# Performance work log

Measured on AMD Instinct MI355X. Metric: run time of the kernel, lower is better.

The kernel has to match this reference:

```python
import jax, jax.numpy as jnp
from jax import lax
import numpy as np

B, C, H, W = 8, 192, 56, 56
N = H * W
K_CLUSTERS = 16   # num_centroids
K_NBRS = 9        # kNN neighbors
FACTOR = 2
COUT = C * FACTOR # hidden channels of graph conv
CPE_K = 7         # depthwise CPE kernel (odd)


def setup_inputs() -> dict:
    key = jax.random.key(0)
    ks = jax.random.split(key, 12)
    s = 0.02
    return {
        "x": jax.random.normal(ks[0], (B, C, H, W), jnp.float32),
        "labels": jax.random.randint(ks[1], (B, N), 0, K_CLUSTERS, jnp.int32),
        "cpe_w": jax.random.normal(ks[2], (C, 1, CPE_K, CPE_K), jnp.float32) * s,
        "cpe_b": jnp.zeros((C,), jnp.float32),
        "fc1_w": jax.random.normal(ks[3], (C, C), jnp.float32) * s,
        "fc1_b": jnp.zeros((C,), jnp.float32),
        "nn_v_w": jax.random.normal(ks[4], (2 * C, COUT), jnp.float32) * s,
        "nn_v_b": jnp.zeros((COUT,), jnp.float32),
        "nn_c_w": jax.random.normal(ks[5], (2 * C, COUT), jnp.float32) * s,
        "nn_c_b": jnp.zeros((COUT,), jnp.float32),
        "fc2_w": jax.random.normal(ks[6], (COUT, C), jnp.float32) * s,
        "fc2_b": jnp.zeros((C,), jnp.float32),
    }


def reference(x, labels, cpe_w, cpe_b, fc1_w, fc1_b, nn_v_w, nn_v_b,
              nn_c_w, nn_c_b, fc2_w, fc2_b):
    Bx, Cx, Hx, Wx = x.shape
    n = Hx * Wx
    shortcut = x
    # --- Conditional Position Encoding: depthwise conv + residual ---
    pe = lax.conv_general_dilated(
        x, cpe_w, (1, 1), "SAME", feature_group_count=Cx,
        dimension_numbers=("NCHW", "OIHW", "NCHW"))
    x = pe + cpe_b[None, :, None, None] + x
    # --- fc1: 1x1 conv ---
    xf = jnp.einsum("bchw,cd->bdhw", x, fc1_w) + fc1_b[None, :, None, None]
    xn = xf.reshape(Bx, Cx, n).transpose(0, 2, 1)  # [B,N,C]
    # --- organize_and_map: stable sort nodes by cluster label ---
    order = jnp.argsort(labels, axis=1)            # sorted pos -> orig idx (stable)
    mapping = jnp.argsort(order, axis=1)           # orig idx -> sorted pos
    xs = jnp.take_along_axis(xn, order[:, :, None], axis=1)  # [B,N,C]
    ls = jnp.take_along_axis(labels, order, axis=1)          # [B,N]
    # --- kNN on l2-normalized feats, restricted to same cluster ---
    xe = xs / jnp.maximum(jnp.linalg.norm(xs, axis=-1, keepdims=True), 1e-12)
    sq = jnp.sum(xe * xe, axis=-1)                 # [B,N]
    d2 = sq[:, :, None] + sq[:, None, :] - 2.0 * jnp.einsum("bnc,bmc->bnm", xe, xe)
    same = ls[:, :, None] == ls[:, None, :]        # [B,N,N] cluster mask
    d2 = jnp.where(same, d2, jnp.inf)
    _, nbr = lax.top_k(-d2, K_NBRS)                # [B,N,k] nearest in-cluster
    valid = jnp.take_along_axis(same, nbr, axis=2) # False when cluster < k
    # --- vertex edge conv: max_j MLP([x_i, x_j - x_i]) ---
    xj = jax.vmap(lambda xb, nb: xb[nb])(xs, nbr)  # [B,N,k,C]
    xi = xs[:, :, None, :]
    msg = jnp.concatenate([jnp.broadcast_to(xi, xj.shape), xj - xi], axis=-1)
    h = jax.nn.gelu(msg @ nn_v_w + nn_v_b)         # [B,N,k,COUT]
    h = jnp.where(valid[..., None], h, -jnp.inf)   # self is always valid
    hv = jnp.max(h, axis=2)                        # [B,N,COUT]
    # --- centroid edge conv over cluster centers (fully connected per image) ---
    onehot = (ls[:, :, None] == jnp.arange(K_CLUSTERS)[None, None, :]).astype(xs.dtype)
    cnt = jnp.maximum(onehot.sum(axis=1), 1.0)     # [B,K]
    cen = jnp.einsum("bnk,bnc->bkc", onehot, xs) / cnt[:, :, None]
    ci = cen[:, :, None, :]
    cj = cen[:, None, :, :]
    cmsg = jnp.concatenate(
        [jnp.broadcast_to(ci, (Bx, K_CLUSTERS, K_CLUSTERS, Cx)), cj - ci], axis=-1)
    hc = jnp.max(jax.nn.gelu(cmsg @ nn_c_w + nn_c_b), axis=2)  # [B,K,COUT]
    hcn = jax.vmap(lambda hb, lb: hb[lb])(hc, ls)  # scatter center feat to nodes
    hn = hv + hcn                                  # [B,N,COUT]
    # --- unshuffle back to original raster order ---
    out_nodes = jnp.take_along_axis(hn, mapping[:, :, None], axis=1)
    # --- fc2: 1x1 conv back to C, residual ---
    y = out_nodes @ fc2_w + fc2_b                  # [B,N,C]
    y = y.transpose(0, 2, 1).reshape(Bx, Cx, Hx, Wx)
    return y + shortcut
```

## Files before the change

kernel.cpp:

```cpp
#include <hip/hip_runtime.h>
#include <math.h>

#define NB 8
#define NC 192
#define NH 56
#define NW 56
#define NN 3136
#define NK 16
#define KNB 9
#define NCOUT 384
#define LPMAX 320
#define DSTRIDE 320
#define DSLOT (320 * 320)

#define FLT_INF __builtin_inff()

typedef short s16x8 __attribute__((ext_vector_type(8)));
typedef _Float16 f16x8 __attribute__((ext_vector_type(8)));
typedef float f32x4 __attribute__((ext_vector_type(4)));
typedef unsigned short us8 __attribute__((ext_vector_type(8)));
typedef unsigned short us4 __attribute__((ext_vector_type(4)));

__device__ __forceinline__ float gelu_t(float x) {
    const float k0 = 0.7978845608028654f;
    float u = k0 * (x + 0.044715f * x * x * x);
    float sg = __builtin_amdgcn_rcpf(1.0f + __expf(-2.0f * u));
    return x * sg;
}

__device__ __forceinline__ unsigned short f2bf(float f) {
    unsigned u = __float_as_uint(f);
    u += 0x7fff + ((u >> 16) & 1);
    return (unsigned short)(u >> 16);
}

__device__ __forceinline__ float bf2f(unsigned short h) {
    return __uint_as_float(((unsigned)h) << 16);
}


#define FRONT_CONV_BLOCKS (NB * NC)
#define FRONT_ORDER_BLOCKS (NB * NK)
#define FRONT_WCVT_BLOCKS 288
__global__ __launch_bounds__(256) void front_kernel(
    const float* __restrict__ X, const float* __restrict__ W7, const float* __restrict__ bias,
    unsigned short* __restrict__ xpe,
    const int* __restrict__ labels, int* __restrict__ order, int* __restrict__ mapping,
    int* __restrict__ lsv, int* __restrict__ cntk, int* __restrict__ offk,
    const float* __restrict__ Wf1, const float* __restrict__ Wv, const float* __restrict__ Wf2,
    unsigned short* __restrict__ wf1, unsigned short* __restrict__ wfpmq,
    unsigned short* __restrict__ wfq, unsigned short* __restrict__ wf2) {
    __shared__ float tile[62 * 62];
    __shared__ float wl[49];
    int bid = blockIdx.x;
    int tid = threadIdx.x;
    if (bid < FRONT_CONV_BLOCKS) {
        int bc = (bid & 7) * NC + (bid >> 3);
        int c = bc % NC;
        const float* Xp = X + (size_t)bc * NN;
        if (tid < 49) wl[tid] = W7[(size_t)c * 49 + tid];
        for (int idx = tid; idx < 62 * 62; idx += 256) {
            int ty = idx / 62, tx = idx % 62;
            int gy = ty - 3, gx = tx - 3;
            float v = 0.0f;
            if (gy >= 0 && gy < NH && gx >= 0 && gx < NW) v = Xp[gy * NW + gx];
            tile[idx] = v;
        }
        __syncthreads();
        float cb = bias[c];
        for (int g = tid; g < (NN / 4); g += 256) {
            int y = g / (NW / 4), x0 = (g % (NW / 4)) * 4;
            float a0 = 0.f, a1 = 0.f, a2 = 0.f, a3 = 0.f;
#pragma unroll
            for (int dy = 0; dy < 7; ++dy) {
                const float* tr = &tile[(y + dy) * 62 + x0];
#pragma unroll
                for (int dx = 0; dx < 7; ++dx) {
                    float wv = wl[dy * 7 + dx];
                    a0 += tr[dx] * wv;
                    a1 += tr[dx + 1] * wv;
                    a2 += tr[dx + 2] * wv;
                    a3 += tr[dx + 3] * wv;
                }
            }
            const float* rr = &tile[(y + 3) * 62 + x0 + 3];
            us4 o;
            o[0] = f2bf(a0 + cb + rr[0]);
            o[1] = f2bf(a1 + cb + rr[1]);
            o[2] = f2bf(a2 + cb + rr[2]);
            o[3] = f2bf(a3 + cb + rr[3]);
            *(us4*)(xpe + (size_t)bc * NN + y * NW + x0) = o;
        }
    } else if (bid < FRONT_CONV_BLOCKS + FRONT_ORDER_BLOCKS) {
        if (tid >= 64) return;
        int idx = bid - FRONT_CONV_BLOCKS;
        int b = idx >> 4;
        int k = idx & 15;
        int lane = tid;
        const int* lb = labels + (size_t)b * NN;
        int cntLess = 0, cntEq = 0;
        for (int n0 = 0; n0 < NN; n0 += 64) {
            int lab = lb[n0 + lane] & 15;
            cntLess += __popcll(__ballot(lab < k));
            cntEq += __popcll(__ballot(lab == k));
        }
        int base = cntLess;
        int run = 0;
        for (int n0 = 0; n0 < NN; n0 += 64) {
            int n = n0 + lane;
            int lab = lb[n] & 15;
            bool p = (lab == k);
            unsigned long long mask = __ballot(p);
            int rank = __popcll(mask & ((1ull << lane) - 1ull));
            if (p) {
                int pos = base + run + rank;
                order[b * NN + pos] = n;
                mapping[b * NN + n] = pos;
                lsv[b * NN + pos] = k;
            }
            run += __popcll(mask);
        }
        if (lane == 0) {
            offk[b * NK + k] = base;
            cntk[b * NK + k] = cntEq;
        }
    } else {
        int u = bid - (FRONT_CONV_BLOCKS + FRONT_ORDER_BLOCKS);
        int nt = u % 6, kc = (u / 6) % 12, z = u / 72;
        const float* W;
        unsigned short* Bf;
        int ldw, rowoff, KC, NT;
        bool diff = false;
        if (z == 0) { W = Wf1; Bf = wf1; ldw = NC; rowoff = 0; KC = 6; NT = 3; }
        else if (z == 1) { W = Wv; Bf = wfpmq; ldw = NCOUT; rowoff = 0; KC = 6; NT = 6; diff = true; }
        else if (z == 2) { W = Wv; Bf = wfq; ldw = NCOUT; rowoff = NC; KC = 6; NT = 6; }
        else { W = Wf2; Bf = wf2; ldw = NC; rowoff = 0; KC = 12; NT = 3; }
        if (nt >= NT || kc >= KC) return;
        int c = tid >> 6, l = tid & 63;
        int n = l & 15, q = l >> 4;
        int col = nt * 64 + c * 16 + n;
        int krow = rowoff + kc * 32 + q * 8;
        unsigned short pack[8];
#pragma unroll
        for (int j = 0; j < 8; ++j) {
            float v = W[(size_t)(krow + j) * ldw + col];
            if (diff) v -= W[(size_t)(NC + krow + j) * ldw + col];
            pack[j] = f2bf(v);
        }
        *(us8*)(Bf + ((((size_t)nt * KC + kc) * 4 + c) * 64 + l) * 8) = *(const us8*)pack;
    }
}

__global__ __launch_bounds__(256) void fc1_kernel(const unsigned short* __restrict__ xpe,
                                                  const unsigned short* __restrict__ Bf,
                                                  const float* __restrict__ bias,
                                                  float* __restrict__ xs,
                                                  unsigned short* __restrict__ Cfrag,
                                                  const int* __restrict__ rowmap) {
    int lin = blockIdx.x;
    int b = lin & 7, by = lin >> 3;
    int w = threadIdx.x >> 6, lane = threadIdx.x & 63;
    int sg = by * 4 + w;
    int m = lane & 15, q = lane >> 4;
    int n = by * 64 + w * 16 + m;
    const unsigned short* Xb = xpe + (size_t)b * NC * NN + n;
    f32x4 acc[12] = {};
#pragma unroll
    for (int kc = 0; kc < 6; ++kc) {
        int ch = kc * 32 + q * 8;
        s16x8 a;
#pragma unroll
        for (int j = 0; j < 8; ++j) a[j] = (short)Xb[(size_t)(ch + j) * NN];
#pragma unroll
        for (int ct = 0; ct < 12; ++ct) {
            s16x8 bv = *(const s16x8*)(Bf + ((((size_t)(ct >> 2) * 6 + kc) * 4 + (ct & 3)) * 64 + lane) * 8);
            acc[ct] = __builtin_amdgcn_mfma_f32_16x16x32_bf16(a, bv, acc[ct], 0, 0, 0);
        }
    }
    float* Cb = xs + (size_t)b * NN * NC;
#pragma unroll
    for (int r = 0; r < 4; ++r) {
        int grow = sg * 16 + q * 4 + r;
        int orow = rowmap[(size_t)b * NN + grow];
        int s2 = orow >> 4, m2 = orow & 15;
#pragma unroll
        for (int ct = 0; ct < 12; ++ct) {
            int col = ct * 16 + m;
            float v = acc[ct][r] + bias[col];
            Cb[(size_t)orow * NC + col] = v;
            int kc2 = col >> 5, q2 = (col >> 3) & 3, j2 = col & 7;
            Cfrag[(size_t)b * NN * NC + (((size_t)s2 * 6 + kc2) * 64 + q2 * 16 + m2) * 8 + j2] =
                f2bf(v);
        }
    }
}

template <int KC>
__global__ __launch_bounds__(256) void gemm_mfma_pq(const unsigned short* __restrict__ Af,
                                                    size_t aStride,
                                                    const unsigned short* __restrict__ B1,
                                                    const unsigned short* __restrict__ B2,
                                                    const float* __restrict__ bias,
                                                    unsigned short* __restrict__ PmQ,
                                                    unsigned short* __restrict__ Qh,
                                                    size_t cStride, int ldc) {
    int lin = ((int)blockIdx.z * 49 + blockIdx.y) * 6 + blockIdx.x;
    int b = lin & 7, pos = lin >> 3;
    int bx = pos % 6, by = pos / 6;
    int w = threadIdx.x >> 6, lane = threadIdx.x & 63;
    int sg = by * 4 + w;
    int n0 = bx * 64;
    const unsigned short* Ap = Af + (size_t)b * aStride + ((size_t)sg * KC * 64 + lane) * 8;
    const unsigned short* Bp1 = B1 + ((size_t)bx * KC * 256 + lane) * 8;
    const unsigned short* Bp2 = B2 + ((size_t)bx * KC * 256 + lane) * 8;
    f32x4 acc1[4] = {};
    f32x4 acc2[4] = {};
#pragma unroll
    for (int kc = 0; kc < KC; ++kc) {
        s16x8 a = *(const s16x8*)(Ap + kc * 512);
#pragma unroll
        for (int c = 0; c < 4; ++c) {
            s16x8 b1 = *(const s16x8*)(Bp1 + kc * 2048 + c * 512);
            acc1[c] = __builtin_amdgcn_mfma_f32_16x16x32_bf16(a, b1, acc1[c], 0, 0, 0);
            s16x8 b2 = *(const s16x8*)(Bp2 + kc * 2048 + c * 512);
            acc2[c] = __builtin_amdgcn_mfma_f32_16x16x32_bf16(a, b2, acc2[c], 0, 0, 0);
        }
    }
    int col0 = lane & 15, rq = lane >> 4;
    unsigned short* Pb = PmQ + (size_t)b * cStride;
    unsigned short* Qb = Qh + (size_t)b * cStride;
#pragma unroll
    for (int r = 0; r < 4; ++r) {
        int grow = sg * 16 + rq * 4 + r;
#pragma unroll
        for (int c = 0; c < 4; ++c) {
            int col = n0 + c * 16 + col0;
            Pb[(size_t)grow * ldc + col] = f2bf(acc1[c][r] + bias[col]);
            Qb[(size_t)grow * ldc + col] = f2bf(acc2[c][r]);
        }
    }
}

__global__ __launch_bounds__(384) void xe_cvt_kernel(const float* __restrict__ xs,
                                                     const int* __restrict__ offk,
                                                     const int* __restrict__ cntk,
                                                     _Float16* __restrict__ xef,
                                                     float* __restrict__ sqv) {
    __shared__ float psum[16][25];
    __shared__ float rloc[16];
    int lin = ((int)blockIdx.z * 16 + blockIdx.y) * 20 + blockIdx.x;
    int b = lin & 7, pos = lin >> 3;
    int k = pos / 20, strip = pos % 20;
    int bk = b * NK + k;
    int base = offk[bk], L = cntk[bk];
    if (strip * 16 >= L) return;
    int kc = threadIdx.x >> 6, l = threadIdx.x & 63;
    int m = l & 15, q = l >> 4;
    int rl = strip * 16 + m;
    int row = base + (rl < L ? rl : L - 1);
    const float* src = xs + ((size_t)b * NN + row) * NC + kc * 32 + q * 8;
    float4 v0 = *(const float4*)src;
    float4 v1 = *(const float4*)(src + 4);
    float part = v0.x * v0.x + v0.y * v0.y + v0.z * v0.z + v0.w * v0.w + v1.x * v1.x +
                 v1.y * v1.y + v1.z * v1.z + v1.w * v1.w;
    psum[m][kc * 4 + q] = part;
    __syncthreads();
    if (threadIdx.x < 16) {
        float s = 0.0f;
#pragma unroll
        for (int i2 = 0; i2 < 24; ++i2) s += psum[threadIdx.x][i2];
        float nrm = fmaxf(sqrtf(s), 1e-12f);
        float ri = 1.0f / nrm;
        rloc[threadIdx.x] = ri;
        if (strip * 16 + (int)threadIdx.x < L)
            sqv[(size_t)b * NN + base + strip * 16 + threadIdx.x] = (s * ri) * ri;
    }
    __syncthreads();
    float rv = rloc[m];
    f16x8 pack;
    pack[0] = (_Float16)(v0.x * rv);
    pack[1] = (_Float16)(v0.y * rv);
    pack[2] = (_Float16)(v0.z * rv);
    pack[3] = (_Float16)(v0.w * rv);
    pack[4] = (_Float16)(v1.x * rv);
    pack[5] = (_Float16)(v1.y * rv);
    pack[6] = (_Float16)(v1.z * rv);
    pack[7] = (_Float16)(v1.w * rv);
    *(f16x8*)(xef + (size_t)bk * (20 * 6 * 512) + (((size_t)strip * 6 + kc) * 64 + l) * 8) =
        pack;
}

__global__ __launch_bounds__(256) void gram_kernel(const _Float16* __restrict__ xef,
                                                   const float* __restrict__ sqv,
                                                   const int* __restrict__ offk,
                                                   const int* __restrict__ cntk,
                                                   float* __restrict__ D) {
    int lin = ((int)blockIdx.z * 5 + blockIdx.y) * 5 + blockIdx.x;
    int b = lin & 7, pos = lin >> 3;
    int k = pos / 25, rr = pos % 25;
    int tj = rr / 5, ti = rr % 5;
    int bk = b * NK + k;
    int base = offk[bk], L = cntk[bk];
    if (ti * 64 >= L || tj * 64 >= L) return;
    int w = threadIdx.x >> 6, lane = threadIdx.x & 63;
    const _Float16* Xf = xef + (size_t)bk * (20 * 6 * 512);
    const _Float16* Ap = Xf + (((size_t)(ti * 4 + w) * 6) * 64 + lane) * 8;
    f32x4 acc[4] = {};
#pragma unroll
    for (int kc = 0; kc < 6; ++kc) {
        f16x8 a = *(const f16x8*)(Ap + kc * 512);
#pragma unroll
        for (int js = 0; js < 4; ++js) {
            f16x8 bv = *(const f16x8*)(Xf + (((size_t)(tj * 4 + js) * 6 + kc) * 64 + lane) * 8);
            acc[js] = __builtin_amdgcn_mfma_f32_16x16x32_f16(a, bv, acc[js], 0, 0, 0);
        }
    }
    float* Dr = D + (size_t)bk * DSLOT;
    const float* Sb = sqv + (size_t)b * NN + base;
    int col0 = lane & 15, rq = lane >> 4;
#pragma unroll
    for (int r = 0; r < 4; ++r) {
        int i = ti * 64 + w * 16 + rq * 4 + r;
        if (i >= L) continue;
        float si = Sb[i];
#pragma unroll
        for (int js = 0; js < 4; ++js) {
            int j = tj * 64 + js * 16 + col0;
            if (j < L) Dr[(size_t)i * DSTRIDE + j] = si + Sb[j] - 2.0f * acc[js][r];
        }
    }
}

#define LEXLT(da, ca, db, cb) ((da) < (db) || ((da) == (db) && (ca) < (cb)))
__global__ __launch_bounds__(256) void select9_kernel(const float* __restrict__ D,
                                                      const int* __restrict__ lsv,
                                                      const int* __restrict__ offk,
                                                      const int* __restrict__ cntk,
                                                      int* __restrict__ nbr) {
    int lin = (int)blockIdx.y * 784 + blockIdx.x;
    int b = lin & 7, quad = lin >> 3;
    int r = quad * 4 + (threadIdx.x >> 6);
    int lane = threadIdx.x & 63;
    int k = lsv[(size_t)b * NN + r];
    int bk = b * NK + k;
    int base = offk[bk], L = cntk[bk];
    int Lc = L < LPMAX ? L : LPMAX;
    const float* Dr = D + (size_t)bk * DSLOT + (size_t)(r - base) * DSTRIDE;
    float d0, d1, d2, d3, d4;
    int c0, c1, c2, c3, c4;
    c0 = lane;
    c1 = lane + 64;
    c2 = lane + 128;
    c3 = lane + 192;
    c4 = lane + 256;
    d0 = c0 < Lc ? Dr[c0] : FLT_INF;
    d1 = c1 < Lc ? Dr[c1] : FLT_INF;
    d2 = c2 < Lc ? Dr[c2] : FLT_INF;
    d3 = c3 < Lc ? Dr[c3] : FLT_INF;
    d4 = c4 < Lc ? Dr[c4] : FLT_INF;
#define CS(da, ca, db, cb)                  \
    if (LEXLT(db, cb, da, ca)) {            \
        float t = da; da = db; db = t;      \
        int u = ca; ca = cb; cb = u;        \
    }
    CS(d0, c0, d1, c1) CS(d3, c3, d4, c4) CS(d2, c2, d4, c4) CS(d2, c2, d3, c3)
    CS(d1, c1, d4, c4) CS(d0, c0, d3, c3) CS(d0, c0, d2, c2) CS(d1, c1, d3, c3)
    CS(d1, c1, d2, c2)
#undef CS
    size_t row = (size_t)b * NN + r;
    for (int q = 0; q < KNB; ++q) {
        float bd = d0;
        int bc = c0;
#pragma unroll
        for (int m = 32; m; m >>= 1) {
            float od = __shfl_xor(bd, m, 64);
            int oc = __shfl_xor(bc, m, 64);
            if (LEXLT(od, oc, bd, bc)) {
                bd = od;
                bc = oc;
            }
        }
        if (lane == 0) nbr[row * KNB + q] = base + bc;
        if (d0 == bd && c0 == bc) {
            d0 = d1; c0 = c1;
            d1 = d2; c1 = c2;
            d2 = d3; c2 = c3;
            d3 = d4; c3 = c4;
            d4 = FLT_INF; c4 = 0x7fffffff;
        }
    }
}

__global__ __launch_bounds__(768) void cenpq_kernel(const float* __restrict__ xs,
                                                    const int* __restrict__ offk,
                                                    const int* __restrict__ cntk,
                                                    const float* __restrict__ Wc,
                                                    const float* __restrict__ bc,
                                                    float* __restrict__ Pc,
                                                    float* __restrict__ Qc) {
    __shared__ float part[4][NC];
    __shared__ float ce[NC];
    __shared__ float pcs[NCOUT], qcs[NCOUT];
    int bk = ((int)blockIdx.x & 7) * NK + ((int)blockIdx.x >> 3);
    int b = bk >> 4;
    int base = offk[bk], L = cntk[bk];
    int w = threadIdx.x / NC;
    int c = threadIdx.x % NC;
    const float* Xb = xs + ((size_t)b * NN + base) * NC + c;
    float s = 0.0f;
    for (int r = w; r < L; r += 4) s += Xb[(size_t)r * NC];
    part[w][c] = s;
    __syncthreads();
    if (threadIdx.x < NC) {
        int cc = threadIdx.x;
        float tot = part[0][cc] + part[1][cc] + part[2][cc] + part[3][cc];
        ce[cc] = tot / fmaxf((float)L, 1.0f);
    }
    __syncthreads();
    int o = threadIdx.x % NCOUT, half = threadIdx.x / NCOUT;
    float pc = 0.0f, qc = 0.0f;
    int cs = half * 96, cend = cs + 96;
    for (int c2 = cs; c2 < cend; ++c2) {
        float cv = ce[c2];
        pc += cv * Wc[(size_t)c2 * NCOUT + o];
        qc += cv * Wc[(size_t)(NC + c2) * NCOUT + o];
    }
    if (half == 1) {
        pcs[o] = pc;
        qcs[o] = qc;
    }
    __syncthreads();
    if (half == 0) {
        Pc[(size_t)bk * NCOUT + o] = pc + pcs[o] + bc[o];
        Qc[(size_t)bk * NCOUT + o] = qc + qcs[o];
    }
}

__global__ __launch_bounds__(384) void hcmax_kernel(const float* __restrict__ Pc,
                                                    const float* __restrict__ Qc,
                                                    float* __restrict__ hc) {
    int bk = ((int)blockIdx.x & 7) * NK + ((int)blockIdx.x >> 3);
    int b = bk >> 4, i = bk & 15;
    int o = threadIdx.x;
    float pi = Pc[((size_t)b * NK + i) * NCOUT + o];
    float qi = Qc[((size_t)b * NK + i) * NCOUT + o];
    float pmq = pi - qi;
    float qmn = FLT_INF, qmx = -FLT_INF;
    for (int j = 0; j < NK; ++j) {
        float v = Qc[((size_t)b * NK + j) * NCOUT + o];
        qmn = fminf(qmn, v);
        qmx = fmaxf(qmx, v);
    }
    hc[((size_t)b * NK + i) * NCOUT + o] =
        fmaxf(gelu_t(pmq + qmn), gelu_t(pmq + qmx));
}

__global__ __launch_bounds__(192) void hv_kernel(const unsigned short* __restrict__ PmQ,
                                                 const unsigned short* __restrict__ Qh,
                                                 const int* __restrict__ nbr,
                                                 const int* __restrict__ lsv,
                                                 const float* __restrict__ hc,
                                                 unsigned short* __restrict__ hnf) {
    int lin = (int)blockIdx.y * 784 + blockIdx.x;
    int b = lin & 7, quad = lin >> 3;
    int t = threadIdx.x;
    int rsub = t / 48, c = t % 48;
    int i = quad * 4 + rsub;
    size_t row = (size_t)b * NN + i;
    int lab = lsv[row];
    int o0 = c * 8;
    int jn[KNB];
#pragma unroll
    for (int q = 0; q < KNB; ++q) jn[q] = nbr[row * KNB + q];
    const unsigned short* Qbb = Qh + (size_t)b * NN * NCOUT + o0;
    us8 pv = *(const us8*)(PmQ + row * NCOUT + o0);
    us8 q0 = *(const us8*)(Qbb + (size_t)jn[0] * NCOUT);
    float qmn[8], qmx[8];
#pragma unroll
    for (int e = 0; e < 8; ++e) {
        float v = bf2f(q0[e]);
        qmn[e] = v;
        qmx[e] = v;
    }
#pragma unroll
    for (int q = 1; q < KNB; ++q) {
        us8 qv = *(const us8*)(Qbb + (size_t)jn[q] * NCOUT);
#pragma unroll
        for (int e = 0; e < 8; ++e) {
            float v = bf2f(qv[e]);
            qmn[e] = fminf(qmn[e], v);
            qmx[e] = fmaxf(qmx[e], v);
        }
    }
    const float* hcr = hc + ((size_t)b * NK + lab) * NCOUT + o0;
    float4 h0 = *(const float4*)hcr;
    float4 h1 = *(const float4*)(hcr + 4);
    float hcv[8] = {h0.x, h0.y, h0.z, h0.w, h1.x, h1.y, h1.z, h1.w};
    unsigned short pack[8];
#pragma unroll
    for (int e = 0; e < 8; ++e) {
        float pmq = bf2f(pv[e]);
        float m = fmaxf(gelu_t(pmq + qmn[e]), gelu_t(pmq + qmx[e]));
        pack[e] = f2bf(m + hcv[e]);
    }
    int s = i >> 4, mm = i & 15;
    *(us8*)(hnf + (size_t)b * NN * NCOUT +
            (((size_t)s * 12 + (c >> 2)) * 64 + (c & 3) * 16 + mm) * 8) = *(const us8*)pack;
}

template <int KC>
__global__ __launch_bounds__(256) void gemm_mfma_hb(const unsigned short* __restrict__ Af,
                                                    size_t aStride,
                                                    const unsigned short* __restrict__ Bf,
                                                    const float* __restrict__ bias,
                                                    unsigned short* __restrict__ C,
                                                    size_t cStride, int ldc) {
    int lin = ((int)blockIdx.z * 49 + blockIdx.y) * 3 + blockIdx.x;
    int b = lin & 7, pos = lin >> 3;
    int bx = pos % 3, by = pos / 3;
    int w = threadIdx.x >> 6, lane = threadIdx.x & 63;
    int sg = by * 4 + w;
    int n0 = bx * 64;
    const unsigned short* Ap = Af + (size_t)b * aStride + ((size_t)sg * KC * 64 + lane) * 8;
    const unsigned short* Bp = Bf + ((size_t)bx * KC * 256 + lane) * 8;
    f32x4 acc[4] = {};
#pragma unroll
    for (int kc = 0; kc < KC; ++kc) {
        s16x8 a = *(const s16x8*)(Ap + kc * 512);
#pragma unroll
        for (int c = 0; c < 4; ++c) {
            s16x8 bv = *(const s16x8*)(Bp + kc * 2048 + c * 512);
            acc[c] = __builtin_amdgcn_mfma_f32_16x16x32_bf16(a, bv, acc[c], 0, 0, 0);
        }
    }
    int col0 = lane & 15, rq = lane >> 4;
    unsigned short* Cb = C + (size_t)b * cStride;
#pragma unroll
    for (int r = 0; r < 4; ++r) {
        int grow = sg * 16 + rq * 4 + r;
#pragma unroll
        for (int c = 0; c < 4; ++c) {
            int col = n0 + c * 16 + col0;
            Cb[(size_t)grow * ldc + col] = f2bf(acc[c][r] + bias[col]);
        }
    }
}

__global__ void out_kernel(const unsigned short* __restrict__ T, const float* __restrict__ X,
                           const int* __restrict__ mapping, float* __restrict__ Y) {
    __shared__ float t[32][33];
    int lin = ((int)blockIdx.z * 98 + blockIdx.y) * 6 + blockIdx.x;
    int b = lin & 7, pos = lin >> 3;
    int c0 = (pos % 6) * 32, n0 = (pos / 6) * 32;
    int tx = threadIdx.x, ty = threadIdx.y;
#pragma unroll
    for (int q = 0; q < 4; ++q) {
        int n = n0 + ty + q * 8;
        int srow = mapping[(size_t)b * NN + n];
        t[ty + q * 8][tx] = bf2f(T[((size_t)b * NN + srow) * NC + c0 + tx]);
    }
    __syncthreads();
#pragma unroll
    for (int q = 0; q < 4; ++q) {
        int c = c0 + ty + q * 8;
        size_t idx = ((size_t)b * NC + c) * NN + n0 + tx;
        Y[idx] = t[tx][ty + q * 8] + X[idx];
    }
}

extern "C" void kernel_launch(void* const* d_in, const int* in_sizes, int n_in, void* d_out,
                              int out_size, void* d_ws, size_t ws_size, hipStream_t stream) {
    const float* x = (const float*)d_in[0];
    const int* labels = (const int*)d_in[1];
    const float* cpe_w = (const float*)d_in[2];
    const float* cpe_b = (const float*)d_in[3];
    const float* fc1_w = (const float*)d_in[4];
    const float* fc1_b = (const float*)d_in[5];
    const float* nn_v_w = (const float*)d_in[6];
    const float* nn_v_b = (const float*)d_in[7];
    const float* nn_c_w = (const float*)d_in[8];
    const float* nn_c_b = (const float*)d_in[9];
    const float* fc2_w = (const float*)d_in[10];
    const float* fc2_b = (const float*)d_in[11];
    float* out = (float*)d_out;

    const size_t SZ_XS = (size_t)NB * NN * NC;
    const size_t SZ_P = (size_t)NB * NN * NCOUT;
    const size_t BN = (size_t)NB * NN;
    const size_t SZ_CEN = (size_t)NB * NK * NC;
    const size_t SZ_PC = (size_t)NB * NK * NCOUT;

    float* base = (float*)d_ws;
    float* xs = base;
    float* xpeRegion = xs + SZ_XS;
    float* Pb = xpeRegion + SZ_XS;
    float* Qb = Pb + SZ_P;
    float* rinv = Qb + SZ_P;
    float* sqv = rinv + BN;
    float* cen = sqv + BN;
    float* Pc = cen + SZ_CEN;
    float* Qc = Pc + SZ_PC;
    float* hcv = Qc + SZ_PC;
    int* order = (int*)(hcv + SZ_PC);
    int* mapping = order + BN;
    int* lsv = mapping + BN;
    int* nbrv = lsv + BN;
    int* cntk = nbrv + BN * KNB;
    int* offk = cntk + NB * NK;
    unsigned short* xpe = (unsigned short*)xpeRegion;
    float* Dbuf = Pb;
    unsigned short* PmQh = (unsigned short*)Pb;
    unsigned short* Qh = (unsigned short*)Qb;
    unsigned short* out_t = (unsigned short*)xs;
    unsigned short* frag = (unsigned short*)(offk + NB * NK);
    unsigned short* hn_frag = frag;
    unsigned short* xs_frag = frag + SZ_XS;
    unsigned short* wf1 = frag + 2 * SZ_XS;
    unsigned short* wfpmq = wf1 + (size_t)NC * NC;
    unsigned short* wfq = wfpmq + (size_t)NC * NCOUT;
    unsigned short* wf2 = wfq + (size_t)NC * NCOUT;
    _Float16* xef = (_Float16*)(wf2 + (size_t)NCOUT * NC);

    front_kernel<<<FRONT_CONV_BLOCKS + FRONT_ORDER_BLOCKS + FRONT_WCVT_BLOCKS, 256, 0, stream>>>(
        x, cpe_w, cpe_b, xpe, labels, order, mapping, lsv, cntk, offk, fc1_w, nn_v_w, fc2_w,
        wf1, wfpmq, wfq, wf2);
    fc1_kernel<<<NB * (NN / 64), 256, 0, stream>>>(xpe, wf1, fc1_b, xs, xs_frag, mapping);
    xe_cvt_kernel<<<dim3(LPMAX / 16, NK, NB), 384, 0, stream>>>(xs, offk, cntk, xef, sqv);
    gram_kernel<<<dim3(LPMAX / 64, LPMAX / 64, NB * NK), 256, 0, stream>>>(xef, sqv, offk,
                                                                           cntk, Dbuf);
    select9_kernel<<<dim3(NN / 4, NB), 256, 0, stream>>>(Dbuf, lsv, offk, cntk, nbrv);
    gemm_mfma_pq<6><<<dim3(NCOUT / 64, NN / 64, NB), 256, 0, stream>>>(
        xs_frag, SZ_XS / NB, wfpmq, wfq, nn_v_b, PmQh, Qh, (size_t)NN * NCOUT, NCOUT);
    cenpq_kernel<<<NB * NK, 768, 0, stream>>>(xs, offk, cntk, nn_c_w, nn_c_b, Pc, Qc);
    hcmax_kernel<<<NB * NK, NCOUT, 0, stream>>>(Pc, Qc, hcv);
    hv_kernel<<<dim3(NN / 4, NB), 192, 0, stream>>>(PmQh, Qh, nbrv, lsv, hcv, hn_frag);
    gemm_mfma_hb<12><<<dim3(NC / 64, NN / 64, NB), 256, 0, stream>>>(
        hn_frag, SZ_P / NB, wf2, fc2_b, out_t, (size_t)NN * NC, NC);
    out_kernel<<<dim3(NC / 32, NN / 32, NB), dim3(32, 8), 0, stream>>>(out_t, x, mapping, out);
}
```

Measured before the change: 278.9 us.

## Merge independent middle-stage kernels into three horizontally fused launches

Combines xe_cvt with the centroid P/Q projection, the PQ GEMM with the Gram distance kernel, and the kNN select with the centroid max kernel. Each pair runs in one launch with blockIdx-based dispatch. To make the PQ GEMM and Gram run together, the distance buffer moves out of the P region into a separate workspace area. This removes three launches and inter-kernel gaps and lets independent work fill idle CUs, but needs more workspace and gives heterogeneous blocks sharing one launch_bounds and LDS footprint.

```diff
diff --git a/kernel.cpp b/kernel.cpp
--- a/kernel.cpp
+++ b/kernel.cpp
@@ -195,264 +195,266 @@
     }
 }
 
-template <int KC>
-__global__ __launch_bounds__(256) void gemm_mfma_pq(const unsigned short* __restrict__ Af,
-                                                    size_t aStride,
-                                                    const unsigned short* __restrict__ B1,
-                                                    const unsigned short* __restrict__ B2,
-                                                    const float* __restrict__ bias,
-                                                    unsigned short* __restrict__ PmQ,
-                                                    unsigned short* __restrict__ Qh,
-                                                    size_t cStride, int ldc) {
-    int lin = ((int)blockIdx.z * 49 + blockIdx.y) * 6 + blockIdx.x;
-    int b = lin & 7, pos = lin >> 3;
-    int bx = pos % 6, by = pos / 6;
-    int w = threadIdx.x >> 6, lane = threadIdx.x & 63;
-    int sg = by * 4 + w;
-    int n0 = bx * 64;
-    const unsigned short* Ap = Af + (size_t)b * aStride + ((size_t)sg * KC * 64 + lane) * 8;
-    const unsigned short* Bp1 = B1 + ((size_t)bx * KC * 256 + lane) * 8;
-    const unsigned short* Bp2 = B2 + ((size_t)bx * KC * 256 + lane) * 8;
-    f32x4 acc1[4] = {};
-    f32x4 acc2[4] = {};
-#pragma unroll
-    for (int kc = 0; kc < KC; ++kc) {
-        s16x8 a = *(const s16x8*)(Ap + kc * 512);
-#pragma unroll
-        for (int c = 0; c < 4; ++c) {
-            s16x8 b1 = *(const s16x8*)(Bp1 + kc * 2048 + c * 512);
-            acc1[c] = __builtin_amdgcn_mfma_f32_16x16x32_bf16(a, b1, acc1[c], 0, 0, 0);
-            s16x8 b2 = *(const s16x8*)(Bp2 + kc * 2048 + c * 512);
-            acc2[c] = __builtin_amdgcn_mfma_f32_16x16x32_bf16(a, b2, acc2[c], 0, 0, 0);
-        }
-    }
-    int col0 = lane & 15, rq = lane >> 4;
-    unsigned short* Pb = PmQ + (size_t)b * cStride;
-    unsigned short* Qb = Qh + (size_t)b * cStride;
-#pragma unroll
-    for (int r = 0; r < 4; ++r) {
-        int grow = sg * 16 + rq * 4 + r;
-#pragma unroll
-        for (int c = 0; c < 4; ++c) {
-            int col = n0 + c * 16 + col0;
-            Pb[(size_t)grow * ldc + col] = f2bf(acc1[c][r] + bias[col]);
-            Qb[(size_t)grow * ldc + col] = f2bf(acc2[c][r]);
-        }
-    }
-}
-
-__global__ __launch_bounds__(384) void xe_cvt_kernel(const float* __restrict__ xs,
-                                                     const int* __restrict__ offk,
-                                                     const int* __restrict__ cntk,
-                                                     _Float16* __restrict__ xef,
-                                                     float* __restrict__ sqv) {
+#define MID_XE_BLOCKS 2560
+#define MID_CEN_BLOCKS 128
+__global__ __launch_bounds__(384) void mid_kernel(const float* __restrict__ xs,
+                                                  const int* __restrict__ offk,
+                                                  const int* __restrict__ cntk,
+                                                  _Float16* __restrict__ xef,
+                                                  float* __restrict__ sqv,
+                                                  const float* __restrict__ Wc,
+                                                  const float* __restrict__ bc,
+                                                  float* __restrict__ Pc,
+                                                  float* __restrict__ Qc) {
     __shared__ float psum[16][25];
     __shared__ float rloc[16];
-    int lin = ((int)blockIdx.z * 16 + blockIdx.y) * 20 + blockIdx.x;
-    int b = lin & 7, pos = lin >> 3;
-    int k = pos / 20, strip = pos % 20;
-    int bk = b * NK + k;
-    int base = offk[bk], L = cntk[bk];
-    if (strip * 16 >= L) return;
-    int kc = threadIdx.x >> 6, l = threadIdx.x & 63;
-    int m = l & 15, q = l >> 4;
-    int rl = strip * 16 + m;
-    int row = base + (rl < L ? rl : L - 1);
-    const float* src = xs + ((size_t)b * NN + row) * NC + kc * 32 + q * 8;
-    float4 v0 = *(const float4*)src;
-    float4 v1 = *(const float4*)(src + 4);
-    float part = v0.x * v0.x + v0.y * v0.y + v0.z * v0.z + v0.w * v0.w + v1.x * v1.x +
-                 v1.y * v1.y + v1.z * v1.z + v1.w * v1.w;
-    psum[m][kc * 4 + q] = part;
-    __syncthreads();
-    if (threadIdx.x < 16) {
-        float s = 0.0f;
-#pragma unroll
-        for (int i2 = 0; i2 < 24; ++i2) s += psum[threadIdx.x][i2];
-        float nrm = fmaxf(sqrtf(s), 1e-12f);
-        float ri = 1.0f / nrm;
-        rloc[threadIdx.x] = ri;
-        if (strip * 16 + (int)threadIdx.x < L)
-            sqv[(size_t)b * NN + base + strip * 16 + threadIdx.x] = (s * ri) * ri;
-    }
-    __syncthreads();
-    float rv = rloc[m];
-    f16x8 pack;
-    pack[0] = (_Float16)(v0.x * rv);
-    pack[1] = (_Float16)(v0.y * rv);
-    pack[2] = (_Float16)(v0.z * rv);
-    pack[3] = (_Float16)(v0.w * rv);
-    pack[4] = (_Float16)(v1.x * rv);
-    pack[5] = (_Float16)(v1.y * rv);
-    pack[6] = (_Float16)(v1.z * rv);
-    pack[7] = (_Float16)(v1.w * rv);
-    *(f16x8*)(xef + (size_t)bk * (20 * 6 * 512) + (((size_t)strip * 6 + kc) * 64 + l) * 8) =
-        pack;
-}
-
-__global__ __launch_bounds__(256) void gram_kernel(const _Float16* __restrict__ xef,
-                                                   const float* __restrict__ sqv,
-                                                   const int* __restrict__ offk,
-                                                   const int* __restrict__ cntk,
-                                                   float* __restrict__ D) {
-    int lin = ((int)blockIdx.z * 5 + blockIdx.y) * 5 + blockIdx.x;
-    int b = lin & 7, pos = lin >> 3;
-    int k = pos / 25, rr = pos % 25;
-    int tj = rr / 5, ti = rr % 5;
-    int bk = b * NK + k;
-    int base = offk[bk], L = cntk[bk];
-    if (ti * 64 >= L || tj * 64 >= L) return;
-    int w = threadIdx.x >> 6, lane = threadIdx.x & 63;
-    const _Float16* Xf = xef + (size_t)bk * (20 * 6 * 512);
-    const _Float16* Ap = Xf + (((size_t)(ti * 4 + w) * 6) * 64 + lane) * 8;
-    f32x4 acc[4] = {};
-#pragma unroll
-    for (int kc = 0; kc < 6; ++kc) {
-        f16x8 a = *(const f16x8*)(Ap + kc * 512);
-#pragma unroll
-        for (int js = 0; js < 4; ++js) {
-            f16x8 bv = *(const f16x8*)(Xf + (((size_t)(tj * 4 + js) * 6 + kc) * 64 + lane) * 8);
-            acc[js] = __builtin_amdgcn_mfma_f32_16x16x32_f16(a, bv, acc[js], 0, 0, 0);
-        }
-    }
-    float* Dr = D + (size_t)bk * DSLOT;
-    const float* Sb = sqv + (size_t)b * NN + base;
-    int col0 = lane & 15, rq = lane >> 4;
-#pragma unroll
-    for (int r = 0; r < 4; ++r) {
-        int i = ti * 64 + w * 16 + rq * 4 + r;
-        if (i >= L) continue;
-        float si = Sb[i];
-#pragma unroll
-        for (int js = 0; js < 4; ++js) {
-            int j = tj * 64 + js * 16 + col0;
-            if (j < L) Dr[(size_t)i * DSTRIDE + j] = si + Sb[j] - 2.0f * acc[js][r];
+    __shared__ float part[4][NC];
+    __shared__ float ce[NC];
+    int bid = blockIdx.x;
+    if (bid < MID_XE_BLOCKS) {
+        int lin = bid;
+        int b = lin & 7, pos = lin >> 3;
+        int k = pos / 20, strip = pos % 20;
+        int bk = b * NK + k;
+        int base = offk[bk], L = cntk[bk];
+        if (strip * 16 >= L) return;
+        int kc = threadIdx.x >> 6, l = threadIdx.x & 63;
+        int m = l & 15, q = l >> 4;
+        int rl = strip * 16 + m;
+        int row = base + (rl < L ? rl : L - 1);
+        const float* src = xs + ((size_t)b * NN + row) * NC + kc * 32 + q * 8;
+        float4 v0 = *(const float4*)src;
+        float4 v1 = *(const float4*)(src + 4);
+        float part2 = v0.x * v0.x + v0.y * v0.y + v0.z * v0.z + v0.w * v0.w + v1.x * v1.x +
+                      v1.y * v1.y + v1.z * v1.z + v1.w * v1.w;
+        psum[m][kc * 4 + q] = part2;
+        __syncthreads();
+        if (threadIdx.x < 16) {
+            float s = 0.0f;
+#pragma unroll
+            for (int i2 = 0; i2 < 24; ++i2) s += psum[threadIdx.x][i2];
+            float nrm = fmaxf(sqrtf(s), 1e-12f);
+            float ri = 1.0f / nrm;
+            rloc[threadIdx.x] = ri;
+            if (strip * 16 + (int)threadIdx.x < L)
+                sqv[(size_t)b * NN + base + strip * 16 + threadIdx.x] = (s * ri) * ri;
+        }
+        __syncthreads();
+        float rv = rloc[m];
+        f16x8 pack;
+        pack[0] = (_Float16)(v0.x * rv);
+        pack[1] = (_Float16)(v0.y * rv);
+        pack[2] = (_Float16)(v0.z * rv);
+        pack[3] = (_Float16)(v0.w * rv);
+        pack[4] = (_Float16)(v1.x * rv);
+        pack[5] = (_Float16)(v1.y * rv);
+        pack[6] = (_Float16)(v1.z * rv);
+        pack[7] = (_Float16)(v1.w * rv);
+        *(f16x8*)(xef + (size_t)bk * (20 * 6 * 512) + (((size_t)strip * 6 + kc) * 64 + l) * 8) =
+            pack;
+    } else {
+        int idx = bid - MID_XE_BLOCKS;
+        int bk = ((idx & 7) * NK) + (idx >> 3);
+        int b = bk >> 4;
+        int base = offk[bk], L = cntk[bk];
+        int c = threadIdx.x % NC;
+        int w2 = threadIdx.x / NC;
+        const float* Xb = xs + ((size_t)b * NN + base) * NC + c;
+        float s0 = 0.0f, s1 = 0.0f;
+        for (int r = w2; r < L; r += 4) s0 += Xb[(size_t)r * NC];
+        for (int r = w2 + 2; r < L; r += 4) s1 += Xb[(size_t)r * NC];
+        part[w2][c] = s0;
+        part[w2 + 2][c] = s1;
+        __syncthreads();
+        if (threadIdx.x < NC) {
+            int cc = threadIdx.x;
+            float tot = part[0][cc] + part[1][cc] + part[2][cc] + part[3][cc];
+            ce[cc] = tot / fmaxf((float)L, 1.0f);
+        }
+        __syncthreads();
+        int o = threadIdx.x;
+        float pcA = 0.0f, qcA = 0.0f, pcB = 0.0f, qcB = 0.0f;
+        for (int c2 = 0; c2 < 96; ++c2) {
+            float cv = ce[c2];
+            pcA += cv * Wc[(size_t)c2 * NCOUT + o];
+            qcA += cv * Wc[(size_t)(NC + c2) * NCOUT + o];
+        }
+        for (int c2 = 96; c2 < 192; ++c2) {
+            float cv = ce[c2];
+            pcB += cv * Wc[(size_t)c2 * NCOUT + o];
+            qcB += cv * Wc[(size_t)(NC + c2) * NCOUT + o];
+        }
+        Pc[(size_t)bk * NCOUT + o] = pcA + pcB + bc[o];
+        Qc[(size_t)bk * NCOUT + o] = qcA + qcB;
+    }
+}
+
+#define L4_PQ_BLOCKS 2352
+#define L4_GRAM_BLOCKS 3200
+__global__ __launch_bounds__(256) void knnpq_kernel(
+    const unsigned short* __restrict__ Af, const unsigned short* __restrict__ B1,
+    const unsigned short* __restrict__ B2, const float* __restrict__ bias,
+    unsigned short* __restrict__ PmQ, unsigned short* __restrict__ Qh,
+    const _Float16* __restrict__ xef, const float* __restrict__ sqv,
+    const int* __restrict__ offk, const int* __restrict__ cntk, float* __restrict__ D) {
+    int bid = blockIdx.x;
+    if (bid < L4_PQ_BLOCKS) {
+        int lin = bid;
+        int b = lin & 7, pos = lin >> 3;
+        int bx = pos % 6, by = pos / 6;
+        int w = threadIdx.x >> 6, lane = threadIdx.x & 63;
+        int sg = by * 4 + w;
+        int n0 = bx * 64;
+        const unsigned short* Ap = Af + (size_t)b * NN * NC + ((size_t)sg * 6 * 64 + lane) * 8;
+        const unsigned short* Bp1 = B1 + ((size_t)bx * 6 * 256 + lane) * 8;
+        const unsigned short* Bp2 = B2 + ((size_t)bx * 6 * 256 + lane) * 8;
+        f32x4 acc1[4] = {};
+        f32x4 acc2[4] = {};
+#pragma unroll
+        for (int kc = 0; kc < 6; ++kc) {
+            s16x8 a = *(const s16x8*)(Ap + kc * 512);
+#pragma unroll
+            for (int c = 0; c < 4; ++c) {
+                s16x8 b1 = *(const s16x8*)(Bp1 + kc * 2048 + c * 512);
+                acc1[c] = __builtin_amdgcn_mfma_f32_16x16x32_bf16(a, b1, acc1[c], 0, 0, 0);
+                s16x8 b2 = *(const s16x8*)(Bp2 + kc * 2048 + c * 512);
+                acc2[c] = __builtin_amdgcn_mfma_f32_16x16x32_bf16(a, b2, acc2[c], 0, 0, 0);
+            }
+        }
+        int col0 = lane & 15, rq = lane >> 4;
+        unsigned short* Pb = PmQ + (size_t)b * NN * NCOUT;
+        unsigned short* Qb = Qh + (size_t)b * NN * NCOUT;
+#pragma unroll
+        for (int r = 0; r < 4; ++r) {
+            int grow = sg * 16 + rq * 4 + r;
+#pragma unroll
+            for (int c = 0; c < 4; ++c) {
+                int col = n0 + c * 16 + col0;
+                Pb[(size_t)grow * NCOUT + col] = f2bf(acc1[c][r] + bias[col]);
+                Qb[(size_t)grow * NCOUT + col] = f2bf(acc2[c][r]);
+            }
+        }
+    } else {
+        int idx = bid - L4_PQ_BLOCKS;
+        int b = idx & 7, pos = idx >> 3;
+        int k = pos / 25, rr = pos % 25;
+        int tj = rr / 5, ti = rr % 5;
+        int bk = b * NK + k;
+        int base = offk[bk], L = cntk[bk];
+        if (ti * 64 >= L || tj * 64 >= L) return;
+        int w = threadIdx.x >> 6, lane = threadIdx.x & 63;
+        const _Float16* Xf = xef + (size_t)bk * (20 * 6 * 512);
+        const _Float16* Ap = Xf + (((size_t)(ti * 4 + w) * 6) * 64 + lane) * 8;
+        f32x4 acc[4] = {};
+#pragma unroll
+        for (int kc = 0; kc < 6; ++kc) {
+            f16x8 a = *(const f16x8*)(Ap + kc * 512);
+#pragma unroll
+            for (int js = 0; js < 4; ++js) {
+                f16x8 bv = *(const f16x8*)(Xf + (((size_t)(tj * 4 + js) * 6 + kc) * 64 + lane) * 8);
+                acc[js] = __builtin_amdgcn_mfma_f32_16x16x32_f16(a, bv, acc[js], 0, 0, 0);
+            }
+        }
+        float* Dr = D + (size_t)bk * DSLOT;
+        const float* Sb = sqv + (size_t)b * NN + base;
+        int col0 = lane & 15, rq = lane >> 4;
+#pragma unroll
+        for (int r = 0; r < 4; ++r) {
+            int i = ti * 64 + w * 16 + rq * 4 + r;
+            if (i >= L) continue;
+            float si = Sb[i];
+#pragma unroll
+            for (int js = 0; js < 4; ++js) {
+                int j = tj * 64 + js * 16 + col0;
+                if (j < L) Dr[(size_t)i * DSTRIDE + j] = si + Sb[j] - 2.0f * acc[js][r];
+            }
         }
     }
 }
 
 #define LEXLT(da, ca, db, cb) ((da) < (db) || ((da) == (db) && (ca) < (cb)))
-__global__ __launch_bounds__(256) void select9_kernel(const float* __restrict__ D,
-                                                      const int* __restrict__ lsv,
-                                                      const int* __restrict__ offk,
-                                                      const int* __restrict__ cntk,
-                                                      int* __restrict__ nbr) {
-    int lin = (int)blockIdx.y * 784 + blockIdx.x;
-    int b = lin & 7, quad = lin >> 3;
-    int r = quad * 4 + (threadIdx.x >> 6);
-    int lane = threadIdx.x & 63;
-    int k = lsv[(size_t)b * NN + r];
-    int bk = b * NK + k;
-    int base = offk[bk], L = cntk[bk];
-    int Lc = L < LPMAX ? L : LPMAX;
-    const float* Dr = D + (size_t)bk * DSLOT + (size_t)(r - base) * DSTRIDE;
-    float d0, d1, d2, d3, d4;
-    int c0, c1, c2, c3, c4;
-    c0 = lane;
-    c1 = lane + 64;
-    c2 = lane + 128;
-    c3 = lane + 192;
-    c4 = lane + 256;
-    d0 = c0 < Lc ? Dr[c0] : FLT_INF;
-    d1 = c1 < Lc ? Dr[c1] : FLT_INF;
-    d2 = c2 < Lc ? Dr[c2] : FLT_INF;
-    d3 = c3 < Lc ? Dr[c3] : FLT_INF;
-    d4 = c4 < Lc ? Dr[c4] : FLT_INF;
+#define L5_SEL_BLOCKS 6272
+#define L5_HC_BLOCKS 128
+__global__ __launch_bounds__(256) void sel_kernel(const float* __restrict__ D,
+                                                  const int* __restrict__ lsv,
+                                                  const int* __restrict__ offk,
+                                                  const int* __restrict__ cntk,
+                                                  int* __restrict__ nbr,
+                                                  const float* __restrict__ Pc,
+                                                  const float* __restrict__ Qc,
+                                                  float* __restrict__ hc) {
+    int bid = blockIdx.x;
+    if (bid < L5_SEL_BLOCKS) {
+        int lin = bid;
+        int b = lin & 7, quad = lin >> 3;
+        int r = quad * 4 + (threadIdx.x >> 6);
+        int lane = threadIdx.x & 63;
+        int k = lsv[(size_t)b * NN + r];
+        int bk = b * NK + k;
+        int base = offk[bk], L = cntk[bk];
+        int Lc = L < LPMAX ? L : LPMAX;
+        const float* Dr = D + (size_t)bk * DSLOT + (size_t)(r - base) * DSTRIDE;
+        float d0, d1, d2, d3, d4;
+        int c0, c1, c2, c3, c4;
+        c0 = lane;
+        c1 = lane + 64;
+        c2 = lane + 128;
+        c3 = lane + 192;
+        c4 = lane + 256;
+        d0 = c0 < Lc ? Dr[c0] : FLT_INF;
+        d1 = c1 < Lc ? Dr[c1] : FLT_INF;
+        d2 = c2 < Lc ? Dr[c2] : FLT_INF;
+        d3 = c3 < Lc ? Dr[c3] : FLT_INF;
+        d4 = c4 < Lc ? Dr[c4] : FLT_INF;
 #define CS(da, ca, db, cb)                  \
     if (LEXLT(db, cb, da, ca)) {            \
         float t = da; da = db; db = t;      \
         int u = ca; ca = cb; cb = u;        \
     }
-    CS(d0, c0, d1, c1) CS(d3, c3, d4, c4) CS(d2, c2, d4, c4) CS(d2, c2, d3, c3)
-    CS(d1, c1, d4, c4) CS(d0, c0, d3, c3) CS(d0, c0, d2, c2) CS(d1, c1, d3, c3)
-    CS(d1, c1, d2, c2)
+        CS(d0, c0, d1, c1) CS(d3, c3, d4, c4) CS(d2, c2, d4, c4) CS(d2, c2, d3, c3)
+        CS(d1, c1, d4, c4) CS(d0, c0, d3, c3) CS(d0, c0, d2, c2) CS(d1, c1, d3, c3)
+        CS(d1, c1, d2, c2)
 #undef CS
-    size_t row = (size_t)b * NN + r;
-    for (int q = 0; q < KNB; ++q) {
-        float bd = d0;
-        int bc = c0;
-#pragma unroll
-        for (int m = 32; m; m >>= 1) {
-            float od = __shfl_xor(bd, m, 64);
-            int oc = __shfl_xor(bc, m, 64);
-            if (LEXLT(od, oc, bd, bc)) {
-                bd = od;
-                bc = oc;
-            }
-        }
-        if (lane == 0) nbr[row * KNB + q] = base + bc;
-        if (d0 == bd && c0 == bc) {
-            d0 = d1; c0 = c1;
-            d1 = d2; c1 = c2;
-            d2 = d3; c2 = c3;
-            d3 = d4; c3 = c4;
-            d4 = FLT_INF; c4 = 0x7fffffff;
-        }
-    }
-}
-
-__global__ __launch_bounds__(768) void cenpq_kernel(const float* __restrict__ xs,
-                                                    const int* __restrict__ offk,
-                                                    const int* __restrict__ cntk,
-                                                    const float* __restrict__ Wc,
-                                                    const float* __restrict__ bc,
-                                                    float* __restrict__ Pc,
-                                                    float* __restrict__ Qc) {
-    __shared__ float part[4][NC];
-    __shared__ float ce[NC];
-    __shared__ float pcs[NCOUT], qcs[NCOUT];
-    int bk = ((int)blockIdx.x & 7) * NK + ((int)blockIdx.x >> 3);
-    int b = bk >> 4;
-    int base = offk[bk], L = cntk[bk];
-    int w = threadIdx.x / NC;
-    int c = threadIdx.x % NC;
-    const float* Xb = xs + ((size_t)b * NN + base) * NC + c;
-    float s = 0.0f;
-    for (int r = w; r < L; r += 4) s += Xb[(size_t)r * NC];
-    part[w][c] = s;
-    __syncthreads();
-    if (threadIdx.x < NC) {
-        int cc = threadIdx.x;
-        float tot = part[0][cc] + part[1][cc] + part[2][cc] + part[3][cc];
-        ce[cc] = tot / fmaxf((float)L, 1.0f);
-    }
-    __syncthreads();
-    int o = threadIdx.x % NCOUT, half = threadIdx.x / NCOUT;
-    float pc = 0.0f, qc = 0.0f;
-    int cs = half * 96, cend = cs + 96;
-    for (int c2 = cs; c2 < cend; ++c2) {
-        float cv = ce[c2];
-        pc += cv * Wc[(size_t)c2 * NCOUT + o];
-        qc += cv * Wc[(size_t)(NC + c2) * NCOUT + o];
-    }
-    if (half == 1) {
-        pcs[o] = pc;
-        qcs[o] = qc;
-    }
-    __syncthreads();
-    if (half == 0) {
-        Pc[(size_t)bk * NCOUT + o] = pc + pcs[o] + bc[o];
-        Qc[(size_t)bk * NCOUT + o] = qc + qcs[o];
-    }
-}
-
-__global__ __launch_bounds__(384) void hcmax_kernel(const float* __restrict__ Pc,
-                                                    const float* __restrict__ Qc,
-                                                    float* __restrict__ hc) {
-    int bk = ((int)blockIdx.x & 7) * NK + ((int)blockIdx.x >> 3);
-    int b = bk >> 4, i = bk & 15;
-    int o = threadIdx.x;
-    float pi = Pc[((size_t)b * NK + i) * NCOUT + o];
-    float qi = Qc[((size_t)b * NK + i) * NCOUT + o];
-    float pmq = pi - qi;
-    float qmn = FLT_INF, qmx = -FLT_INF;
-    for (int j = 0; j < NK; ++j) {
-        float v = Qc[((size_t)b * NK + j) * NCOUT + o];
-        qmn = fminf(qmn, v);
-        qmx = fmaxf(qmx, v);
-    }
-    hc[((size_t)b * NK + i) * NCOUT + o] =
-        fmaxf(gelu_t(pmq + qmn), gelu_t(pmq + qmx));
+        size_t row = (size_t)b * NN + r;
+        for (int q = 0; q < KNB; ++q) {
+            float bd = d0;
+            int bc = c0;
+#pragma unroll
+            for (int m = 32; m; m >>= 1) {
+                float od = __shfl_xor(bd, m, 64);
+                int oc = __shfl_xor(bc, m, 64);
+                if (LEXLT(od, oc, bd, bc)) {
+                    bd = od;
+                    bc = oc;
+                }
+            }
+            if (lane == 0) nbr[row * KNB + q] = base + bc;
+            if (d0 == bd && c0 == bc) {
+                d0 = d1; c0 = c1;
+                d1 = d2; c1 = c2;
+                d2 = d3; c2 = c3;
+                d3 = d4; c3 = c4;
+                d4 = FLT_INF; c4 = 0x7fffffff;
+            }
+        }
+    } else {
+        int idx = bid - L5_SEL_BLOCKS;
+        int bk = ((idx & 7) * NK) + (idx >> 3);
+        int b = bk >> 4, i = bk & 15;
+        for (int o = threadIdx.x; o < NCOUT; o += 256) {
+            float pi = Pc[((size_t)b * NK + i) * NCOUT + o];
+            float qi = Qc[((size_t)b * NK + i) * NCOUT + o];
+            float pmq = pi - qi;
+            float qmn = FLT_INF, qmx = -FLT_INF;
+            for (int j = 0; j < NK; ++j) {
+                float v = Qc[((size_t)b * NK + j) * NCOUT + o];
+                qmn = fminf(qmn, v);
+                qmx = fmaxf(qmx, v);
+            }
+            hc[((size_t)b * NK + i) * NCOUT + o] =
+                fmaxf(gelu_t(pmq + qmn), gelu_t(pmq + qmx));
+        }
+    }
 }
 
 __global__ __launch_bounds__(192) void hv_kernel(const unsigned short* __restrict__ PmQ,
@@ -608,7 +610,6 @@
     int* cntk = nbrv + BN * KNB;
     int* offk = cntk + NB * NK;
     unsigned short* xpe = (unsigned short*)xpeRegion;
-    float* Dbuf = Pb;
     unsigned short* PmQh = (unsigned short*)Pb;
     unsigned short* Qh = (unsigned short*)Qb;
     unsigned short* out_t = (unsigned short*)xs;
@@ -620,19 +621,18 @@
     unsigned short* wfq = wfpmq + (size_t)NC * NCOUT;
     unsigned short* wf2 = wfq + (size_t)NC * NCOUT;
     _Float16* xef = (_Float16*)(wf2 + (size_t)NCOUT * NC);
+    float* Dbuf = (float*)(xef + (size_t)(NB * NK) * (20 * 6 * 512));
 
     front_kernel<<<FRONT_CONV_BLOCKS + FRONT_ORDER_BLOCKS + FRONT_WCVT_BLOCKS, 256, 0, stream>>>(
         x, cpe_w, cpe_b, xpe, labels, order, mapping, lsv, cntk, offk, fc1_w, nn_v_w, fc2_w,
         wf1, wfpmq, wfq, wf2);
     fc1_kernel<<<NB * (NN / 64), 256, 0, stream>>>(xpe, wf1, fc1_b, xs, xs_frag, mapping);
-    xe_cvt_kernel<<<dim3(LPMAX / 16, NK, NB), 384, 0, stream>>>(xs, offk, cntk, xef, sqv);
-    gram_kernel<<<dim3(LPMAX / 64, LPMAX / 64, NB * NK), 256, 0, stream>>>(xef, sqv, offk,
-                                                                           cntk, Dbuf);
-    select9_kernel<<<dim3(NN / 4, NB), 256, 0, stream>>>(Dbuf, lsv, offk, cntk, nbrv);
-    gemm_mfma_pq<6><<<dim3(NCOUT / 64, NN / 64, NB), 256, 0, stream>>>(
-        xs_frag, SZ_XS / NB, wfpmq, wfq, nn_v_b, PmQh, Qh, (size_t)NN * NCOUT, NCOUT);
-    cenpq_kernel<<<NB * NK, 768, 0, stream>>>(xs, offk, cntk, nn_c_w, nn_c_b, Pc, Qc);
-    hcmax_kernel<<<NB * NK, NCOUT, 0, stream>>>(Pc, Qc, hcv);
+    mid_kernel<<<MID_XE_BLOCKS + MID_CEN_BLOCKS, 384, 0, stream>>>(
+        xs, offk, cntk, xef, sqv, nn_c_w, nn_c_b, Pc, Qc);
+    knnpq_kernel<<<L4_PQ_BLOCKS + L4_GRAM_BLOCKS, 256, 0, stream>>>(
+        xs_frag, wfpmq, wfq, nn_v_b, PmQh, Qh, xef, sqv, offk, cntk, Dbuf);
+    sel_kernel<<<L5_SEL_BLOCKS + L5_HC_BLOCKS, 256, 0, stream>>>(
+        Dbuf, lsv, offk, cntk, nbrv, Pc, Qc, hcv);
     hv_kernel<<<dim3(NN / 4, NB), 192, 0, stream>>>(PmQh, Qh, nbrv, lsv, hcv, hn_frag);
     gemm_mfma_hb<12><<<dim3(NC / 64, NN / 64, NB), 256, 0, stream>>>(
         hn_frag, SZ_P / NB, wf2, fc2_b, out_t, (size_t)NN * NC, NC);
```

Measured after the change: 267.4 us. 4.1% less time.
